# Optimization experiments

Measured on AMD Instinct MI355X. Metric: run time of the kernel, lower is better.

The kernel has to match this reference:

```python
import jax, jax.numpy as jnp
import numpy as np

C_IN, C_INT = 256, 128


def setup_inputs() -> dict:
    key = jax.random.key(0)
    ks = jax.random.split(key, 7)
    B, H, W = 8, 64, 64
    s_in = 1.0 / np.sqrt(C_IN)
    return {
        "x": jax.random.normal(ks[0], (B, C_IN, H, W), dtype=jnp.float32),
        "w_theta": jax.random.uniform(ks[1], (C_INT, C_IN), jnp.float32, -s_in, s_in),
        "b_theta": jax.random.uniform(ks[2], (C_INT,), jnp.float32, -s_in, s_in),
        "w_phi": jax.random.uniform(ks[3], (C_INT, C_IN), jnp.float32, -s_in, s_in),
        "b_phi": jax.random.uniform(ks[4], (C_INT,), jnp.float32, -s_in, s_in),
        "w_g": jax.random.uniform(ks[5], (C_INT, C_IN), jnp.float32, -s_in, s_in),
        "b_g": jax.random.uniform(ks[6], (C_INT,), jnp.float32, -s_in, s_in),
    }


def reference(x, w_theta, b_theta, w_phi, b_phi, w_g, b_g):
    B, C, H, W = x.shape
    # flatten spatial: [B, N, C], 1x1 conv == per-position linear
    xf = x.reshape(B, C, H * W).transpose(0, 2, 1)  # [B, N, C_in]
    theta = jnp.einsum('bnc,dc->bnd', xf, w_theta) + b_theta  # [B, N, C_int]
    phi = jnp.einsum('bnc,dc->bnd', xf, w_phi) + b_phi        # [B, N, C_int]
    g = jnp.einsum('bnc,dc->bnd', xf, w_g) + b_g              # [B, N, C_int]
    f = jnp.einsum('bnd,bmd->bnm', theta, phi)  # [B, N, N] unscaled scores
    f_div_C = jax.nn.softmax(f, axis=-1)
    y = jnp.einsum('bnm,bmd->bnd', f_div_C, g)  # [B, N, C_int]
    # back to [B, C_int, H, W]
    return y.transpose(0, 2, 1).reshape(B, C_INT, H, W)
```

## Files before the change

### kernel.cpp

```cpp
#include <hip/hip_runtime.h>

typedef __attribute__((ext_vector_type(8))) short bf8;
typedef __attribute__((ext_vector_type(4))) float f4;
typedef unsigned short u16;

constexpr int B_ = 8, CIN = 256, CINT = 128, NN = 4096;
constexpr float L2E = 1.44269504088896f;

__device__ __forceinline__ u16 f2bf(float f) {
  unsigned int u = __builtin_bit_cast(unsigned int, f);
  u += 0x7FFFu + ((u >> 16) & 1u);
  return (u16)(u >> 16);
}

__device__ __forceinline__ void glds16(const void* g, void* l) {
  __builtin_amdgcn_global_load_lds(
      (const __attribute__((address_space(1))) unsigned int*)g,
      (__attribute__((address_space(3))) unsigned int*)l, 16, 0, 0);
}

__global__ __launch_bounds__(256) void prep_kernel(
    const float* __restrict__ wth, const float* __restrict__ wph,
    const float* __restrict__ wg, u16* __restrict__ wbf)
{
  int i = blockIdx.x * 256 + threadIdx.x;
  const float* src = (i < 32768) ? wth : (i < 65536) ? wph : wg;
  wbf[i] = f2bf(src[i & 32767]);
}

__global__ __launch_bounds__(256) void proj_kernel(
    const float* __restrict__ x, const u16* __restrict__ wbf,
    const float* __restrict__ bth, const float* __restrict__ bph,
    const float* __restrict__ bg,
    u16* __restrict__ theta, u16* __restrict__ phiT, u16* __restrict__ gTt)
{
  const int b = blockIdx.y, n0 = blockIdx.x * 64;
  const int tid = threadIdx.x, w = tid >> 6, l = tid & 63;
  const int lr = l & 15, lg = l >> 4;
  __shared__ __align__(16) u16 sx[64 * 256];

  const float* xb = x + (size_t)b * CIN * NN + n0;
  #pragma unroll
  for (int pass = 0; pass < 8; ++pass) {
    const int cb = w * 8 + pass * 32;
    u16 tmp[8];
    #pragma unroll
    for (int i = 0; i < 8; ++i) tmp[i] = f2bf(xb[(size_t)(cb + i) * NN + l]);
    uint4 v;
    v.x = (unsigned)tmp[0] | ((unsigned)tmp[1] << 16);
    v.y = (unsigned)tmp[2] | ((unsigned)tmp[3] << 16);
    v.z = (unsigned)tmp[4] | ((unsigned)tmp[5] << 16);
    v.w = (unsigned)tmp[6] | ((unsigned)tmp[7] << 16);
    *(uint4*)&sx[l * 256 + (((w + pass * 4) ^ (l & 7)) << 3)] = v;
  }
  __syncthreads();

  #pragma unroll
  for (int dti = 0; dti < 6; ++dti) {
    const int dt = w * 6 + dti;
    const int mat = dt >> 3, d0 = (dt & 7) * 16;
    const float* Bv = (mat == 0) ? bth : (mat == 1) ? bph : bg;
    const u16* wrow = wbf + mat * 32768 + (size_t)(d0 + lr) * 256 + lg * 8;
    bf8 wf[8];
    #pragma unroll
    for (int ks = 0; ks < 8; ++ks) wf[ks] = *(const bf8*)(wrow + ks * 32);

    #pragma unroll
    for (int mt = 0; mt < 4; ++mt) {
      f4 acc = {0.f, 0.f, 0.f, 0.f};
      const int row = mt * 16 + lr;
      #pragma unroll
      for (int ks = 0; ks < 8; ++ks) {
        bf8 bx = *(const bf8*)&sx[row * 256 + (((ks * 4 + lg) ^ (lr & 7)) << 3)];
        acc = __builtin_amdgcn_mfma_f32_16x16x32_bf16(wf[ks], bx, acc, 0, 0, 0);
      }
      const int m = n0 + mt * 16 + lr;
      const int dlo = d0 + lg * 4;
      if (mat == 0) {
        ushort4 h4;
        h4.x = f2bf(acc[0] + Bv[dlo + 0]);
        h4.y = f2bf(acc[1] + Bv[dlo + 1]);
        h4.z = f2bf(acc[2] + Bv[dlo + 2]);
        h4.w = f2bf(acc[3] + Bv[dlo + 3]);
        *(ushort4*)&theta[((size_t)b * NN + m) * CINT + dlo] = h4;
      } else if (mat == 1) {
        const int kt = m >> 6, rr = m & 63;
        ushort4 h4;
        h4.x = f2bf((acc[0] + Bv[dlo + 0]) * L2E);
        h4.y = f2bf((acc[1] + Bv[dlo + 1]) * L2E);
        h4.z = f2bf((acc[2] + Bv[dlo + 2]) * L2E);
        h4.w = f2bf((acc[3] + Bv[dlo + 3]) * L2E);
        *(ushort4*)&phiT[((size_t)(b * 64 + kt)) * 8192 + rr * 128 +
                         ((((dlo >> 3) ^ (rr & 7))) << 3) + (dlo & 7)] = h4;
      } else {
        const int kt = m >> 6, rr = m & 63;
        #pragma unroll
        for (int r = 0; r < 4; ++r) {
          const int d = dlo + r;
          gTt[((size_t)(b * 64 + kt)) * 8192 + d * 64 +
              (((rr >> 3) ^ (d & 7)) << 3) + (rr & 7)] = f2bf(acc[r] + Bv[d]);
        }
      }
    }
  }
}

__global__ __launch_bounds__(512, 2) void attn_kernel(
    const u16* __restrict__ theta, const u16* __restrict__ phiT,
    const u16* __restrict__ gTt, float* __restrict__ out)
{
  const int b  = blockIdx.y;
  const int t_ = threadIdx.x;
  const int w  = t_ >> 6;
  const int l  = t_ & 63;
  const int lr = l & 15, lg = l >> 4;
  const int h  = w >> 2, wq = w & 3;
  const int qw = blockIdx.x * 128 + wq * 32;

  __shared__ __align__(16) u16 sphi[2][2][64 * 128];
  __shared__ __align__(16) u16 sg[2][2][128 * 64];
  __shared__ __align__(16) u16 sP[8][16 * 64];

  const u16* th = theta + (size_t)b * NN * CINT;

  bf8 qf[2][4];
  #pragma unroll
  for (int qt = 0; qt < 2; ++qt)
    #pragma unroll
    for (int ds = 0; ds < 4; ++ds)
      qf[qt][ds] = *(const bf8*)(th + (size_t)(qw + qt * 16 + lr) * CINT + ds * 32 + lg * 8);

  f4 y[2][8];
  #pragma unroll
  for (int qt = 0; qt < 2; ++qt)
    #pragma unroll
    for (int dt = 0; dt < 8; ++dt) y[qt][dt] = (f4){0.f, 0.f, 0.f, 0.f};
  float rs[2] = {0.f, 0.f};

  const char* pph = (const char*)(phiT + (size_t)(b * 64 + h * 32) * 8192) +
                    wq * 4096 + l * 16;
  const char* pgg = (const char*)(gTt + (size_t)(b * 64 + h * 32) * 8192) +
                    wq * 4096 + l * 16;

  #define STAGE(BUF)                                                     \
    {                                                                    \
      char* lp = (char*)&sphi[h][BUF][0] + wq * 4096;                    \
      char* lq = (char*)&sg[h][BUF][0] + wq * 4096;                      \
      glds16(pph, lp);        glds16(pph + 1024, lp + 1024);             \
      glds16(pph + 2048, lp + 2048); glds16(pph + 3072, lp + 3072);      \
      glds16(pgg, lq);        glds16(pgg + 1024, lq + 1024);             \
      glds16(pgg + 2048, lq + 2048); glds16(pgg + 3072, lq + 3072);      \
      pph += 16384; pgg += 16384;                                        \
    }

  STAGE(0);
  __syncthreads();
  int cur = 0;

  for (int t = 0; t < 32; ++t) {
    if (t < 31) STAGE(cur ^ 1);

    f4 s[2][4];
    #pragma unroll
    for (int qt = 0; qt < 2; ++qt)
      #pragma unroll
      for (int st = 0; st < 4; ++st) s[qt][st] = (f4){0.f, 0.f, 0.f, 0.f};
    __builtin_amdgcn_s_setprio(1);
    #pragma unroll
    for (int st = 0; st < 4; ++st) {
      const u16* base = &sphi[h][cur][(st * 16 + lr) * 128];
      #pragma unroll
      for (int ds = 0; ds < 4; ++ds) {
        bf8 af = *(const bf8*)(base + (((ds * 4 + lg) ^ (lr & 7)) * 8));
        #pragma unroll
        for (int qt = 0; qt < 2; ++qt)
          s[qt][st] = __builtin_amdgcn_mfma_f32_16x16x32_bf16(af, qf[qt][ds], s[qt][st], 0, 0, 0);
      }
    }
    __builtin_amdgcn_s_setprio(0);

    bf8 gfr[8][2];
    #pragma unroll
    for (int dt = 0; dt < 8; ++dt)
      #pragma unroll
      for (int ks = 0; ks < 2; ++ks)
        gfr[dt][ks] = *(const bf8*)&sg[h][cur][(dt * 16 + lr) * 64 + (((ks * 4 + lg) ^ (lr & 7)) * 8)];

    #pragma unroll
    for (int qt = 0; qt < 2; ++qt) {
      #pragma unroll
      for (int st = 0; st < 4; ++st) {
        float p0 = __builtin_amdgcn_exp2f(s[qt][st][0]);
        float p1 = __builtin_amdgcn_exp2f(s[qt][st][1]);
        float p2 = __builtin_amdgcn_exp2f(s[qt][st][2]);
        float p3 = __builtin_amdgcn_exp2f(s[qt][st][3]);
        rs[qt] += (p0 + p1) + (p2 + p3);
        ushort4 pk;
        pk.x = f2bf(p0); pk.y = f2bf(p1); pk.z = f2bf(p2); pk.w = f2bf(p3);
        *(ushort4*)&sP[w][lr * 64 + (((st * 2 + (lg >> 1)) ^ (lr & 7)) << 3) + ((lg & 1) << 2)] = pk;
      }
      bf8 paf[2];
      #pragma unroll
      for (int ks = 0; ks < 2; ++ks)
        paf[ks] = *(const bf8*)&sP[w][lr * 64 + ((((ks << 2) + lg) ^ (lr & 7)) << 3)];
      __builtin_amdgcn_s_setprio(1);
      #pragma unroll
      for (int dt = 0; dt < 8; ++dt) {
        y[qt][dt] = __builtin_amdgcn_mfma_f32_16x16x32_bf16(paf[0], gfr[dt][0], y[qt][dt], 0, 0, 0);
        y[qt][dt] = __builtin_amdgcn_mfma_f32_16x16x32_bf16(paf[1], gfr[dt][1], y[qt][dt], 0, 0, 0);
      }
      __builtin_amdgcn_s_setprio(0);
    }

    __syncthreads();
    cur ^= 1;
  }

  float* ycomb  = (float*)&sphi[0][0][0];
  float* rscomb = (float*)&sg[0][0][0];
  if (h == 1) {
    #pragma unroll
    for (int qt = 0; qt < 2; ++qt) {
      #pragma unroll
      for (int dt = 0; dt < 8; ++dt)
        *(f4*)&ycomb[wq * 4096 + (qt * 8 + dt) * 256 + l * 4] = y[qt][dt];
      rscomb[wq * 128 + qt * 64 + l] = rs[qt];
    }
  }
  __syncthreads();
  if (h == 0) {
    #pragma unroll
    for (int qt = 0; qt < 2; ++qt) {
      #pragma unroll
      for (int dt = 0; dt < 8; ++dt)
        y[qt][dt] += *(const f4*)&ycomb[wq * 4096 + (qt * 8 + dt) * 256 + l * 4];
      rs[qt] += rscomb[wq * 128 + qt * 64 + l];
      rs[qt] += __shfl_xor(rs[qt], 16);
      rs[qt] += __shfl_xor(rs[qt], 32);
    }
    float* ob = out + (size_t)b * CINT * NN;
    #pragma unroll
    for (int qt = 0; qt < 2; ++qt) {
      f4 rsi;
      #pragma unroll
      for (int r = 0; r < 4; ++r)
        rsi[r] = 1.0f / __shfl(rs[qt], lg * 4 + r, 64);
      #pragma unroll
      for (int dt = 0; dt < 8; ++dt) {
        f4 v = y[qt][dt] * rsi;
        *(float4*)&ob[(size_t)(dt * 16 + lr) * NN + qw + qt * 16 + lg * 4] = *(float4*)&v;
      }
    }
  }
}

extern "C" void kernel_launch(void* const* d_in, const int* in_sizes, int n_in,
                              void* d_out, int out_size, void* d_ws, size_t ws_size,
                              hipStream_t stream) {
  const float* x   = (const float*)d_in[0];
  const float* wth = (const float*)d_in[1];
  const float* bth = (const float*)d_in[2];
  const float* wph = (const float*)d_in[3];
  const float* bph = (const float*)d_in[4];
  const float* wg  = (const float*)d_in[5];
  const float* bg  = (const float*)d_in[6];
  float* out = (float*)d_out;

  u16* theta = (u16*)d_ws;
  u16* phiT  = theta + (size_t)B_ * NN * CINT;
  u16* gTt   = phiT  + (size_t)B_ * NN * CINT;
  u16* wbf   = gTt   + (size_t)B_ * NN * CINT;

  hipLaunchKernelGGL(prep_kernel, dim3(384), dim3(256), 0, stream, wth, wph, wg, wbf);
  hipLaunchKernelGGL(proj_kernel, dim3(64, 8), dim3(256), 0, stream,
                     x, wbf, bth, bph, bg, theta, phiT, gTt);
  hipLaunchKernelGGL(attn_kernel, dim3(32, 8), dim3(512), 0, stream,
                     theta, phiT, gTt, out);
}
```

Measured before the change: 123.7 us.

## Use 32-key tiles with triple-buffered LDS staging and vmcnt-based waits

After: 118.1 us. 4.5% less time.

```diff
diff --git a/kernel.cpp b/kernel.cpp
--- a/kernel.cpp
+++ b/kernel.cpp
@@ -84,21 +84,21 @@
         h4.w = f2bf(acc[3] + Bv[dlo + 3]);
         *(ushort4*)&theta[((size_t)b * NN + m) * CINT + dlo] = h4;
       } else if (mat == 1) {
-        const int kt = m >> 6, rr = m & 63;
+        const int kt = m >> 5, r32 = m & 31;
         ushort4 h4;
         h4.x = f2bf((acc[0] + Bv[dlo + 0]) * L2E);
         h4.y = f2bf((acc[1] + Bv[dlo + 1]) * L2E);
         h4.z = f2bf((acc[2] + Bv[dlo + 2]) * L2E);
         h4.w = f2bf((acc[3] + Bv[dlo + 3]) * L2E);
-        *(ushort4*)&phiT[((size_t)(b * 64 + kt)) * 8192 + rr * 128 +
-                         ((((dlo >> 3) ^ (rr & 7))) << 3) + (dlo & 7)] = h4;
+        *(ushort4*)&phiT[((size_t)(b * 128 + kt)) * 4096 + r32 * 128 +
+                         ((((dlo >> 3) ^ (r32 & 7))) << 3) + (dlo & 7)] = h4;
       } else {
-        const int kt = m >> 6, rr = m & 63;
+        const int kt = m >> 5, kk = m & 31;
         #pragma unroll
         for (int r = 0; r < 4; ++r) {
           const int d = dlo + r;
-          gTt[((size_t)(b * 64 + kt)) * 8192 + d * 64 +
-              (((rr >> 3) ^ (d & 7)) << 3) + (rr & 7)] = f2bf(acc[r] + Bv[d]);
+          gTt[((size_t)(b * 128 + kt)) * 4096 + d * 32 +
+              (((kk >> 3) ^ (d & 3)) << 3) + (kk & 7)] = f2bf(acc[r] + Bv[d]);
         }
       }
     }
@@ -117,12 +117,12 @@
   const int h  = w >> 2, wq = w & 3;
   const int qw = blockIdx.x * 128 + wq * 32;
 
-  __shared__ __align__(16) u16 sphi[2][2][64 * 128];
-  __shared__ __align__(16) u16 sg[2][2][128 * 64];
-  __shared__ __align__(16) u16 sP[8][16 * 64];
+  __shared__ __align__(16) char smem[106496];
+  u16* sphi_base = (u16*)smem;
+  u16* sg_base   = (u16*)(smem + 49152);
+  u16* sPw       = (u16*)(smem + 98304 + w * 1024);
 
   const u16* th = theta + (size_t)b * NN * CINT;
-
   bf8 qf[2][4];
   #pragma unroll
   for (int qt = 0; qt < 2; ++qt)
@@ -137,87 +137,93 @@
     for (int dt = 0; dt < 8; ++dt) y[qt][dt] = (f4){0.f, 0.f, 0.f, 0.f};
   float rs[2] = {0.f, 0.f};
 
-  const char* pph = (const char*)(phiT + (size_t)(b * 64 + h * 32) * 8192) +
-                    wq * 4096 + l * 16;
-  const char* pgg = (const char*)(gTt + (size_t)(b * 64 + h * 32) * 8192) +
-                    wq * 4096 + l * 16;
-
-  #define STAGE(BUF)                                                     \
+  const char* psrc = (const char*)(phiT + (size_t)(b * 128 + h * 64) * 4096);
+  const char* gsrc = (const char*)(gTt + (size_t)(b * 128 + h * 64) * 4096);
+
+  #define STAGE(BUF, T)                                                  \
     {                                                                    \
-      char* lp = (char*)&sphi[h][BUF][0] + wq * 4096;                    \
-      char* lq = (char*)&sg[h][BUF][0] + wq * 4096;                      \
-      glds16(pph, lp);        glds16(pph + 1024, lp + 1024);             \
-      glds16(pph + 2048, lp + 2048); glds16(pph + 3072, lp + 3072);      \
-      glds16(pgg, lq);        glds16(pgg + 1024, lq + 1024);             \
-      glds16(pgg + 2048, lq + 2048); glds16(pgg + 3072, lq + 3072);      \
-      pph += 16384; pgg += 16384;                                        \
-    }
-
-  STAGE(0);
+      const char* sp = psrc + (size_t)(T) * 8192 + wq * 2048 + l * 16;   \
+      const char* sq = gsrc + (size_t)(T) * 8192 + wq * 2048 + l * 16;   \
+      char* lp = (char*)(sphi_base + (h * 3 + (BUF)) * 4096) + wq * 2048;\
+      char* lq = (char*)(sg_base + (h * 3 + (BUF)) * 4096) + wq * 2048;  \
+      glds16(sp, lp); glds16(sp + 1024, lp + 1024);                      \
+      glds16(sq, lq); glds16(sq + 1024, lq + 1024);                      \
+    }
+
+  constexpr int NT = 64;
+  STAGE(0, 0);
+  STAGE(1, 1);
+
+  int bc = 0, bs = 2;
+  for (int t = 0; t < NT; ++t) {
+    if (t == NT - 1) asm volatile("s_waitcnt vmcnt(0)" ::: "memory");
+    else             asm volatile("s_waitcnt vmcnt(4)" ::: "memory");
+    __builtin_amdgcn_s_barrier();
+    __builtin_amdgcn_sched_barrier(0);
+
+    if (t < NT - 2) STAGE(bs, t + 2);
+
+    const u16* PH = sphi_base + (h * 3 + bc) * 4096;
+    const u16* GG = sg_base + (h * 3 + bc) * 4096;
+
+    f4 s[2][2];
+    s[0][0] = (f4){0.f,0.f,0.f,0.f}; s[0][1] = (f4){0.f,0.f,0.f,0.f};
+    s[1][0] = (f4){0.f,0.f,0.f,0.f}; s[1][1] = (f4){0.f,0.f,0.f,0.f};
+    __builtin_amdgcn_s_setprio(1);
+    #pragma unroll
+    for (int st = 0; st < 2; ++st) {
+      const u16* base = PH + (st * 16 + lr) * 128;
+      #pragma unroll
+      for (int ds = 0; ds < 4; ++ds) {
+        bf8 af = *(const bf8*)(base + (((ds * 4 + lg) ^ (lr & 7)) << 3));
+        s[0][st] = __builtin_amdgcn_mfma_f32_16x16x32_bf16(af, qf[0][ds], s[0][st], 0, 0, 0);
+        s[1][st] = __builtin_amdgcn_mfma_f32_16x16x32_bf16(af, qf[1][ds], s[1][st], 0, 0, 0);
+      }
+    }
+    __builtin_amdgcn_s_setprio(0);
+
+    bf8 gfr[8];
+    #pragma unroll
+    for (int dt = 0; dt < 8; ++dt)
+      gfr[dt] = *(const bf8*)(GG + (dt * 16 + lr) * 32 + ((lg ^ (lr & 3)) << 3));
+
+    #pragma unroll
+    for (int qt = 0; qt < 2; ++qt) {
+      float p0 = __builtin_amdgcn_exp2f(s[qt][0][0]);
+      float p1 = __builtin_amdgcn_exp2f(s[qt][0][1]);
+      float p2 = __builtin_amdgcn_exp2f(s[qt][0][2]);
+      float p3 = __builtin_amdgcn_exp2f(s[qt][0][3]);
+      float p4 = __builtin_amdgcn_exp2f(s[qt][1][0]);
+      float p5 = __builtin_amdgcn_exp2f(s[qt][1][1]);
+      float p6 = __builtin_amdgcn_exp2f(s[qt][1][2]);
+      float p7 = __builtin_amdgcn_exp2f(s[qt][1][3]);
+      rs[qt] += ((p0 + p1) + (p2 + p3)) + ((p4 + p5) + (p6 + p7));
+      ushort4 pk;
+      pk.x = f2bf(p0); pk.y = f2bf(p1); pk.z = f2bf(p2); pk.w = f2bf(p3);
+      *(ushort4*)&sPw[lr * 32 + (((lg >> 1) ^ (lr & 3)) << 3) + ((lg & 1) << 2)] = pk;
+      pk.x = f2bf(p4); pk.y = f2bf(p5); pk.z = f2bf(p6); pk.w = f2bf(p7);
+      *(ushort4*)&sPw[lr * 32 + (((2 + (lg >> 1)) ^ (lr & 3)) << 3) + ((lg & 1) << 2)] = pk;
+
+      bf8 paf = *(const bf8*)&sPw[lr * 32 + ((lg ^ (lr & 3)) << 3)];
+      __builtin_amdgcn_s_setprio(1);
+      #pragma unroll
+      for (int dt = 0; dt < 8; ++dt)
+        y[qt][dt] = __builtin_amdgcn_mfma_f32_16x16x32_bf16(paf, gfr[dt], y[qt][dt], 0, 0, 0);
+      __builtin_amdgcn_s_setprio(0);
+    }
+
+    bc = (bc == 2) ? 0 : bc + 1;
+    bs = (bs == 2) ? 0 : bs + 1;
+  }
+
+  #pragma unroll
+  for (int qt = 0; qt < 2; ++qt) {
+    rs[qt] += __shfl_xor(rs[qt], 16);
+    rs[qt] += __shfl_xor(rs[qt], 32);
+  }
   __syncthreads();
-  int cur = 0;
-
-  for (int t = 0; t < 32; ++t) {
-    if (t < 31) STAGE(cur ^ 1);
-
-    f4 s[2][4];
-    #pragma unroll
-    for (int qt = 0; qt < 2; ++qt)
-      #pragma unroll
-      for (int st = 0; st < 4; ++st) s[qt][st] = (f4){0.f, 0.f, 0.f, 0.f};
-    __builtin_amdgcn_s_setprio(1);
-    #pragma unroll
-    for (int st = 0; st < 4; ++st) {
-      const u16* base = &sphi[h][cur][(st * 16 + lr) * 128];
-      #pragma unroll
-      for (int ds = 0; ds < 4; ++ds) {
-        bf8 af = *(const bf8*)(base + (((ds * 4 + lg) ^ (lr & 7)) * 8));
-        #pragma unroll
-        for (int qt = 0; qt < 2; ++qt)
-          s[qt][st] = __builtin_amdgcn_mfma_f32_16x16x32_bf16(af, qf[qt][ds], s[qt][st], 0, 0, 0);
-      }
-    }
-    __builtin_amdgcn_s_setprio(0);
-
-    bf8 gfr[8][2];
-    #pragma unroll
-    for (int dt = 0; dt < 8; ++dt)
-      #pragma unroll
-      for (int ks = 0; ks < 2; ++ks)
-        gfr[dt][ks] = *(const bf8*)&sg[h][cur][(dt * 16 + lr) * 64 + (((ks * 4 + lg) ^ (lr & 7)) * 8)];
-
-    #pragma unroll
-    for (int qt = 0; qt < 2; ++qt) {
-      #pragma unroll
-      for (int st = 0; st < 4; ++st) {
-        float p0 = __builtin_amdgcn_exp2f(s[qt][st][0]);
-        float p1 = __builtin_amdgcn_exp2f(s[qt][st][1]);
-        float p2 = __builtin_amdgcn_exp2f(s[qt][st][2]);
-        float p3 = __builtin_amdgcn_exp2f(s[qt][st][3]);
-        rs[qt] += (p0 + p1) + (p2 + p3);
-        ushort4 pk;
-        pk.x = f2bf(p0); pk.y = f2bf(p1); pk.z = f2bf(p2); pk.w = f2bf(p3);
-        *(ushort4*)&sP[w][lr * 64 + (((st * 2 + (lg >> 1)) ^ (lr & 7)) << 3) + ((lg & 1) << 2)] = pk;
-      }
-      bf8 paf[2];
-      #pragma unroll
-      for (int ks = 0; ks < 2; ++ks)
-        paf[ks] = *(const bf8*)&sP[w][lr * 64 + ((((ks << 2) + lg) ^ (lr & 7)) << 3)];
-      __builtin_amdgcn_s_setprio(1);
-      #pragma unroll
-      for (int dt = 0; dt < 8; ++dt) {
-        y[qt][dt] = __builtin_amdgcn_mfma_f32_16x16x32_bf16(paf[0], gfr[dt][0], y[qt][dt], 0, 0, 0);
-        y[qt][dt] = __builtin_amdgcn_mfma_f32_16x16x32_bf16(paf[1], gfr[dt][1], y[qt][dt], 0, 0, 0);
-      }
-      __builtin_amdgcn_s_setprio(0);
-    }
-
-    __syncthreads();
-    cur ^= 1;
-  }
-
-  float* ycomb  = (float*)&sphi[0][0][0];
-  float* rscomb = (float*)&sg[0][0][0];
+  float* ycomb  = (float*)smem;
+  float* rscomb = (float*)(smem + 65536);
   if (h == 1) {
     #pragma unroll
     for (int qt = 0; qt < 2; ++qt) {
@@ -235,8 +241,6 @@
       for (int dt = 0; dt < 8; ++dt)
         y[qt][dt] += *(const f4*)&ycomb[wq * 4096 + (qt * 8 + dt) * 256 + l * 4];
       rs[qt] += rscomb[wq * 128 + qt * 64 + l];
-      rs[qt] += __shfl_xor(rs[qt], 16);
-      rs[qt] += __shfl_xor(rs[qt], 32);
     }
     float* ob = out + (size_t)b * CINT * NN;
     #pragma unroll
```
